# Performance work log

Hardware: AMD Instinct MI355X
Metric: run time of the kernel (lower is better)

## Reference

```python
import jax, jax.numpy as jnp
import numpy as np

DEGREE = 3        # self.degree = 3 in MGNN
K = 3             # Chebyshev/polynomial order of the GCN
BANDWIDTH = 512.0 # Gaussian kernel bandwidth (~2*d so adj spans (0,1])
B, N, D_IN = 2, 4096, 256
D_OUT = 64        # 2*D_OUT == 128 == linear output dim


def _bspline(t, degree):
    """Cox-de Boor recursive B-spline basis N_{0,degree}(t), elementwise,
    uniform knots on [0,1]. t: [B,N,N] adjacency values."""
    knots = np.linspace(0.0, 1.0, degree + 2)  # static python floats
    basis = [jnp.where((t >= knots[i]) & (t < knots[i + 1]), 1.0, 0.0).astype(t.dtype)
             for i in range(degree + 1)]
    for k in range(1, degree + 1):
        basis = [
            (t - knots[i]) / (knots[i + k] - knots[i]) * basis[i]
            + (knots[i + k + 1] - t) / (knots[i + k + 1] - knots[i + 1]) * basis[i + 1]
            for i in range(degree + 1 - k)
        ]
    return basis[0]


def _wavelet(t, degree):
    # spline wavelet: difference of dilated/shifted B-splines
    return _bspline(2.0 * t, degree) - _bspline(2.0 * t - 1.0, degree)


def _graph_construction(x, bandwidth):
    # Gaussian-kernel dense adjacency per batch element: [B,N,N], values in (0,1]
    sq = jnp.sum(x * x, axis=-1)                                   # [B,N]
    d2 = sq[:, :, None] + sq[:, None, :] - 2.0 * jnp.einsum('bnd,bmd->bnm', x, x)
    d2 = jnp.maximum(d2, 0.0)
    return jnp.exp(-d2 / bandwidth)


def _gcn(x, kernel, Wk):
    # out = sum_k (kernel^k x) W_k ; Wk: [K, D_IN, D_OUT]
    h = x
    out = jnp.einsum('bnd,do->bno', h, Wk[0])
    for k in range(1, Wk.shape[0]):
        h = jnp.einsum('bnm,bmd->bnd', kernel, h)
        out = out + jnp.einsum('bnd,do->bno', h, Wk[k])
    return out


def setup_inputs() -> dict:
    key = jax.random.key(0)
    k0, k1, k2, k3 = jax.random.split(key, 4)
    x = jax.random.normal(k0, (B, N, D_IN), dtype=jnp.float32)
    Wk = jax.random.normal(k1, (K, D_IN, D_OUT), dtype=jnp.float32) * 0.05
    W_lin = jax.random.normal(k2, (D_IN, 2 * D_OUT), dtype=jnp.float32) * 0.05
    b_lin = jnp.zeros((2 * D_OUT,), dtype=jnp.float32)
    return {"x": x, "Wk": Wk, "W_lin": W_lin, "b_lin": b_lin}


def reference(x, Wk, W_lin, b_lin):
    adj = _graph_construction(x, BANDWIDTH)       # [B,N,N]
    b_kernel = _bspline(adj, DEGREE)              # [B,N,N]
    w_kernel = _wavelet(adj, DEGREE)              # [B,N,N]
    gcn1 = _gcn(x, b_kernel, Wk)                  # [B,N,D_OUT]
    gcn2 = _gcn(x, w_kernel, Wk)                  # [B,N,D_OUT]
    akgcn = jnp.concatenate([gcn1, gcn2], axis=-1)        # [B,N,2*D_OUT]
    akgcn = jax.nn.relu(akgcn + x @ W_lin + b_lin)        # residual + relu
    return akgcn.reshape(akgcn.shape[0], -1)              # flatten last two dims
```

## Files before the change

kernel.cpp:

```cpp
#include <hip/hip_runtime.h>
#include <hip/hip_bf16.h>

typedef __hip_bfloat16 bf16;
typedef float v4f __attribute__((ext_vector_type(4)));
typedef short v8s __attribute__((ext_vector_type(8)));

typedef const __attribute__((address_space(1))) void gvoid;
typedef __attribute__((address_space(3))) void lvoid;

__device__ __forceinline__ void async16(const void* g, void* l) {
  __builtin_amdgcn_global_load_lds((gvoid*)g, (lvoid*)l, 16, 0, 0);
}

__device__ __forceinline__ unsigned short f2bf(float v) {
  __hip_bfloat16 h = __float2bfloat16(v);
  return *(unsigned short*)&h;
}
__device__ __forceinline__ float bflo(unsigned dw) {
  unsigned u = dw << 16;
  return *(float*)&u;
}
__device__ __forceinline__ float bfhi(unsigned dw) {
  unsigned u = dw & 0xffff0000u;
  return *(float*)&u;
}

__device__ __forceinline__ float b3(float u) {
  u = fminf(fmaxf(u, 0.f), 4.f);
  float t1 = fmaxf(u - 1.f, 0.f);
  float t2 = fmaxf(u - 2.f, 0.f);
  float t3 = fmaxf(u - 3.f, 0.f);
  float c0 = u * u * u;
  float c1 = t1 * t1 * t1;
  float c2 = t2 * t2 * t2;
  float c3 = t3 * t3 * t3;
  return (c0 - 4.f * c1 + 6.f * c2 - 4.f * c3) * (1.f / 6.f);
}

template <int NI, int BK>
__device__ __forceinline__ void mfma_loop(const bf16* __restrict__ A,
                                          const bf16* __restrict__ B, int lda,
                                          int ldb, int kLen, bf16* As, bf16* Bs,
                                          v4f acc[4][NI]) {
  const int tid = threadIdx.x;
  const int wave = tid >> 6;
  const int lane = tid & 63;
  const int quad = lane >> 4;
  const int r16 = lane & 15;
  const int wm = (wave >> 1) * 64;
  const int wn = (wave & 1) * (NI * 16);
  constexpr int CPR = BK / 8;
  constexpr int AQ = 128 * CPR / 256;
  constexpr int BQ = NI * 32 * CPR / 256;
  char* AsC = (char*)As;
  char* BsC = (char*)Bs;
  for (int kk = 0; kk < kLen; kk += BK) {
#pragma unroll
    for (int q = 0; q < AQ; ++q) {
      const int ch = tid + 256 * q;
      const int r = ch / CPR, c = (ch % CPR) * 8;
      async16(A + (size_t)r * lda + kk + c, AsC + q * 4096 + wave * 1024);
    }
#pragma unroll
    for (int q = 0; q < BQ; ++q) {
      const int ch = tid + 256 * q;
      const int r = ch / CPR, c = (ch % CPR) * 8;
      async16(B + (size_t)r * ldb + kk + c, BsC + q * 4096 + wave * 1024);
    }
    __syncthreads();
#pragma unroll
    for (int ks = 0; ks < BK / 32; ++ks) {
      v8s af[4], bfr[NI];
#pragma unroll
      for (int mi = 0; mi < 4; ++mi)
        af[mi] =
            *(const v8s*)(As + (wm + mi * 16 + r16) * BK + ks * 32 + quad * 8);
#pragma unroll
      for (int ni = 0; ni < NI; ++ni)
        bfr[ni] =
            *(const v8s*)(Bs + (wn + ni * 16 + r16) * BK + ks * 32 + quad * 8);
#pragma unroll
      for (int mi = 0; mi < 4; ++mi)
#pragma unroll
        for (int ni = 0; ni < NI; ++ni)
          acc[mi][ni] = __builtin_amdgcn_mfma_f32_16x16x32_bf16(
              af[mi], bfr[ni], acc[mi][ni], 0, 0, 0);
    }
    __syncthreads();
  }
}

__global__ void prep(const float* __restrict__ x, bf16* __restrict__ U,
                     float* __restrict__ sq) {
  const int n = blockIdx.x, b = blockIdx.y, t = threadIdx.x;
  const size_t row = (size_t)b * 4096 + n;
  float v = x[row * 256 + t];
  U[row * 1280 + t] = __float2bfloat16(v);
  float s = v * v;
#pragma unroll
  for (int o = 32; o > 0; o >>= 1) s += __shfl_down(s, o, 64);
  __shared__ float ls[4];
  if ((t & 63) == 0) ls[t >> 6] = s;
  __syncthreads();
  if (t == 0) sq[row] = ls[0] + ls[1] + ls[2] + ls[3];
}

__global__ void transk(const float* __restrict__ src, bf16* __restrict__ dst) {
  __shared__ float tile[64][65];
  const int z = blockIdx.z;
  const float* s = src + (size_t)z * 4096 * 256;
  bf16* d = dst + (size_t)z * 256 * 4096;
  const int n0 = blockIdx.x * 64, d0 = blockIdx.y * 64;
  const int tx = threadIdx.x & 31, ty = threadIdx.x >> 5;
#pragma unroll
  for (int i = 0; i < 8; ++i) {
    const int r = ty + i * 8;
    const float2 v = *(const float2*)(s + (size_t)(n0 + r) * 256 + d0 + tx * 2);
    tile[r][tx * 2] = v.x;
    tile[r][tx * 2 + 1] = v.y;
  }
  __syncthreads();
#pragma unroll
  for (int i = 0; i < 8; ++i) {
    const int c = ty + i * 8;
    __hip_bfloat162 p;
    p.x = __float2bfloat16(tile[tx * 2][c]);
    p.y = __float2bfloat16(tile[tx * 2 + 1][c]);
    *(__hip_bfloat162*)(d + (size_t)(d0 + c) * 4096 + n0 + tx * 2) = p;
  }
}

__global__ void wbig(const float* __restrict__ Wk, const float* __restrict__ Wl,
                     bf16* __restrict__ WbT) {
  int idx = blockIdx.x * 256 + threadIdx.x;
  if (idx >= 128 * 1280) return;
  int j = idx / 1280, k = idx % 1280;
  int o = j & 63;
  float v = 0.f;
  if (k < 256)
    v = Wk[k * 64 + o] + Wl[k * 128 + j];
  else if (k < 512)
    v = (j < 64) ? Wk[16384 + (k - 256) * 64 + o] : 0.f;
  else if (k < 768)
    v = (j < 64) ? Wk[32768 + (k - 512) * 64 + o] : 0.f;
  else if (k < 1024)
    v = (j >= 64) ? Wk[16384 + (k - 768) * 64 + o] : 0.f;
  else
    v = (j >= 64) ? Wk[32768 + (k - 1024) * 64 + o] : 0.f;
  WbT[idx] = __float2bfloat16(v);
}

__global__ __launch_bounds__(256, 2) void gemm_s(const bf16* __restrict__ U,
                                                 const float* __restrict__ sq,
                                                 bf16* __restrict__ kmat) {
  __shared__ __align__(16) bf16 As[128 * 64];
  __shared__ __align__(16) bf16 Bs[128 * 64];
  __shared__ unsigned lut[2048];
  const int tid = threadIdx.x;
  for (int i = tid; i < 2048; i += 256) {
    float t = (i + 0.5f) * (1.f / 2048.f);
    float bv = b3(4.f * t);
    float wv = b3(8.f * t) - b3(8.f * t - 4.f);
    lut[i] = (unsigned)f2bf(bv) | ((unsigned)f2bf(wv) << 16);
  }
  const int z = blockIdx.z;
  const bf16* A = U + (size_t)z * 4096 * 1280 + (size_t)blockIdx.x * 128 * 1280;
  const bf16* B = U + (size_t)z * 4096 * 1280 + (size_t)blockIdx.y * 128 * 1280;
  v4f acc[4][4];
#pragma unroll
  for (int a = 0; a < 4; ++a)
#pragma unroll
    for (int b2 = 0; b2 < 4; ++b2) acc[a][b2] = (v4f){0.f, 0.f, 0.f, 0.f};
  mfma_loop<4, 64>(A, B, 1280, 1280, 256, As, Bs, acc);
  const int wave = tid >> 6, lane = tid & 63;
  const int quad = lane >> 4, r16 = lane & 15;
  const int wm = (wave >> 1) * 64, wn = (wave & 1) * 64;
  const float* sqr = sq + (size_t)z * 4096;
  unsigned short* bk = (unsigned short*)(kmat + (size_t)(z * 2) * 4096 * 4096);
  unsigned short* wk = bk + (size_t)4096 * 4096;
  const int i0 = blockIdx.x * 128 + wm + quad * 4;
  const int j0 = blockIdx.y * 128 + wn + r16;
  const int par = lane & 1;
  const int jc = j0 - par;
  float sqj[4];
#pragma unroll
  for (int ni = 0; ni < 4; ++ni) sqj[ni] = sqr[j0 + ni * 16];
  const float c = -1.4426950408889634f / 512.f;
#pragma unroll
  for (int mi = 0; mi < 4; ++mi) {
#pragma unroll
    for (int ni = 0; ni < 4; ++ni) {
      unsigned pv[4];
#pragma unroll
      for (int r = 0; r < 4; ++r) {
        float s = acc[mi][ni][r];
        float d2 = fmaxf(sqr[i0 + mi * 16 + r] + sqj[ni] - 2.f * s, 0.f);
        float t = __builtin_amdgcn_exp2f(d2 * c);
        int idx = (int)fminf(t * 2048.f, 2047.f);
        pv[r] = lut[idx];
      }
      unsigned ov[4];
#pragma unroll
      for (int r = 0; r < 4; ++r) ov[r] = __shfl_xor((int)pv[r], 1, 64);
#pragma unroll
      for (int rr = 0; rr < 2; ++rr) {
        const int r = par * 2 + rr;
        const unsigned a = pv[r], b2 = ov[r];
        const unsigned lo = par ? b2 : a;
        const unsigned hi = par ? a : b2;
        const unsigned bkd = (lo & 0xffffu) | (hi << 16);
        const unsigned wkd = (lo >> 16) | (hi & 0xffff0000u);
        const int i = i0 + mi * 16 + r;
        const size_t off = (size_t)i * 4096 + jc + ni * 16;
        *(unsigned*)(bk + off) = bkd;
        *(unsigned*)(wk + off) = wkd;
      }
    }
  }
}

__global__ __launch_bounds__(256, 4) void gemm_h(const bf16* __restrict__ kmat,
                                                 const bf16* __restrict__ BtBase,
                                                 bf16* __restrict__ hpart,
                                                 int btShift) {
  __shared__ __align__(16) bf16 As[128 * 64];
  __shared__ __align__(16) bf16 Bs[128 * 64];
  const int bz = blockIdx.z;
  const int z = bz >> 2, split = bz & 3;
  const int kk0 = split * 1024;
  const bf16* A =
      kmat + (size_t)z * 4096 * 4096 + (size_t)blockIdx.x * 128 * 4096 + kk0;
  const bf16* B = BtBase + (size_t)(z >> btShift) * 256 * 4096 +
                  (size_t)blockIdx.y * 128 * 4096 + kk0;
  v4f acc[4][4];
#pragma unroll
  for (int a = 0; a < 4; ++a)
#pragma unroll
    for (int b2 = 0; b2 < 4; ++b2) acc[a][b2] = (v4f){0.f, 0.f, 0.f, 0.f};
  mfma_loop<4, 64>(A, B, 4096, 4096, 1024, As, Bs, acc);
  const int tid = threadIdx.x, wave = tid >> 6, lane = tid & 63;
  const int quad = lane >> 4, r16 = lane & 15;
  const int wm = (wave >> 1) * 64, wn = (wave & 1) * 64;
  bf16* H = hpart + ((size_t)split * 4 + z) * 4096 * 256;
  const int i0 = blockIdx.x * 128 + wm + quad * 4;
  const int j0 = blockIdx.y * 128 + wn + r16;
  const int par = lane & 1;
  const int jc = j0 - par;
#pragma unroll
  for (int mi = 0; mi < 4; ++mi) {
#pragma unroll
    for (int ni = 0; ni < 4; ++ni) {
      unsigned pv[4];
#pragma unroll
      for (int r = 0; r < 4; ++r) pv[r] = (unsigned)f2bf(acc[mi][ni][r]);
      unsigned ov[4];
#pragma unroll
      for (int r = 0; r < 4; ++r) ov[r] = __shfl_xor((int)pv[r], 1, 64);
#pragma unroll
      for (int rr = 0; rr < 2; ++rr) {
        const int r = par * 2 + rr;
        const unsigned a = pv[r], b2 = ov[r];
        const unsigned lo = par ? b2 : a;
        const unsigned hi = par ? a : b2;
        const int i = i0 + mi * 16 + r;
        *(unsigned*)(H + (size_t)i * 256 + jc + ni * 16) = lo | (hi << 16);
      }
    }
  }
}

__global__ void reduceT(const bf16* __restrict__ hpart, bf16* __restrict__ U,
                        bf16* __restrict__ hT, int uoffBase) {
  __shared__ float tile[64][65];
  const int z = blockIdx.z;
  const int b = z >> 1, kern = z & 1;
  const int uoff = uoffBase + kern * 512;
  const int n0 = blockIdx.x * 64, d0 = blockIdx.y * 64;
  const int tx = threadIdx.x & 31, ty = threadIdx.x >> 5;
  const size_t sstride = (size_t)4 * 4096 * 256;
  const bf16* s0 = hpart + (size_t)z * 4096 * 256;
#pragma unroll
  for (int i = 0; i < 8; ++i) {
    const int r = ty + i * 8;
    const size_t off = (size_t)(n0 + r) * 256 + d0 + tx * 2;
    float vx = 0.f, vy = 0.f;
#pragma unroll
    for (int k = 0; k < 4; ++k) {
      const unsigned dw = *(const unsigned*)(s0 + k * sstride + off);
      vx += bflo(dw);
      vy += bfhi(dw);
    }
    tile[r][tx * 2] = vx;
    tile[r][tx * 2 + 1] = vy;
    __hip_bfloat162 p;
    p.x = __float2bfloat16(vx);
    p.y = __float2bfloat16(vy);
    *(__hip_bfloat162*)(U + (size_t)(b * 4096 + n0 + r) * 1280 + uoff + d0 +
                        tx * 2) = p;
  }
  if (hT) {
    __syncthreads();
#pragma unroll
    for (int i = 0; i < 8; ++i) {
      const int c = ty + i * 8;
      __hip_bfloat162 p;
      p.x = __float2bfloat16(tile[tx * 2][c]);
      p.y = __float2bfloat16(tile[tx * 2 + 1][c]);
      *(__hip_bfloat162*)(hT + (size_t)z * 256 * 4096 + (size_t)(d0 + c) * 4096 +
                          n0 + tx * 2) = p;
    }
  }
}

__global__ __launch_bounds__(256, 4) void gemm_proj(
    const bf16* __restrict__ U, const bf16* __restrict__ WbT,
    const float* __restrict__ blin, float* __restrict__ out) {
  __shared__ __align__(16) bf16 As[128 * 64];
  __shared__ __align__(16) bf16 Bs[64 * 64];
  const bf16* A = U + (size_t)blockIdx.x * 128 * 1280;
  const bf16* B = WbT + (size_t)blockIdx.y * 64 * 1280;
  v4f acc[4][2];
#pragma unroll
  for (int a = 0; a < 4; ++a)
#pragma unroll
    for (int b2 = 0; b2 < 2; ++b2) acc[a][b2] = (v4f){0.f, 0.f, 0.f, 0.f};
  mfma_loop<2, 64>(A, B, 1280, 1280, 1280, As, Bs, acc);
  const int tid = threadIdx.x, wave = tid >> 6, lane = tid & 63;
  const int quad = lane >> 4, r16 = lane & 15;
  const int wm = (wave >> 1) * 64, wn = (wave & 1) * 32;
  const int i0 = blockIdx.x * 128 + wm + quad * 4;
  const int j0 = blockIdx.y * 64 + wn + r16;
#pragma unroll
  for (int mi = 0; mi < 4; ++mi)
#pragma unroll
    for (int r = 0; r < 4; ++r) {
      const int i = i0 + mi * 16 + r;
#pragma unroll
      for (int ni = 0; ni < 2; ++ni) {
        const int j = j0 + ni * 16;
        out[(size_t)i * 128 + j] = fmaxf(acc[mi][ni][r] + blin[j], 0.f);
      }
    }
}

extern "C" void kernel_launch(void* const* d_in, const int* in_sizes, int n_in,
                              void* d_out, int out_size, void* d_ws,
                              size_t ws_size, hipStream_t stream) {
  const float* x = (const float*)d_in[0];
  const float* Wk = (const float*)d_in[1];
  const float* Wlin = (const float*)d_in[2];
  const float* blin = (const float*)d_in[3];
  float* out = (float*)d_out;
  char* w = (char*)d_ws;
  bf16* kmat = (bf16*)(w);
  bf16* hpart = (bf16*)(w + 134217728);
  bf16* h1T = (bf16*)(w + 201326592);
  bf16* xhT = (bf16*)(w + 209715200);
  bf16* U = (bf16*)(w + 213909504);
  bf16* WbT = (bf16*)(w + 234881024);
  float* sqv = (float*)(w + 235208704);

  prep<<<dim3(4096, 2), 256, 0, stream>>>(x, U, sqv);
  transk<<<dim3(64, 4, 2), 256, 0, stream>>>(x, xhT);
  wbig<<<dim3(640), 256, 0, stream>>>(Wk, Wlin, WbT);
  gemm_s<<<dim3(32, 32, 2), 256, 0, stream>>>(U, sqv, kmat);
  gemm_h<<<dim3(32, 2, 16), 256, 0, stream>>>(kmat, xhT, hpart, 1);
  reduceT<<<dim3(64, 4, 4), 256, 0, stream>>>(hpart, U, h1T, 256);
  gemm_h<<<dim3(32, 2, 16), 256, 0, stream>>>(kmat, h1T, hpart, 0);
  reduceT<<<dim3(64, 4, 4), 256, 0, stream>>>(hpart, U, nullptr, 512);
  gemm_proj<<<dim3(64, 2), 256, 0, stream>>>(U, WbT, blin, out);
}
```

Before: 243.7 us.

## Store B-spline and wavelet kernels as packed 8-bit codes and dequantize in GEMM

The adjacency-derived B-spline and wavelet kernel matrices were stored as two bf16 planes. They are now quantized to 8-bit codes, packed into one 16-bit word per element, and written as a single plane. The propagation GEMM loads these words through registers, unpacks and dequantizes them to bf16, and writes them to LDS. This halves kernel-matrix traffic in both the writing kernel and the two reading GEMMs. The costs are coarser precision in the kernel values, extra ALU work per loaded element, and losing the asynchronous LDS load for the A operand.

```diff
diff --git a/kernel.cpp b/kernel.cpp
--- a/kernel.cpp
+++ b/kernel.cpp
@@ -4,6 +4,7 @@
 typedef __hip_bfloat16 bf16;
 typedef float v4f __attribute__((ext_vector_type(4)));
 typedef short v8s __attribute__((ext_vector_type(8)));
+typedef unsigned u32;
 
 typedef const __attribute__((address_space(1))) void gvoid;
 typedef __attribute__((address_space(3))) void lvoid;
@@ -16,12 +17,12 @@
   __hip_bfloat16 h = __float2bfloat16(v);
   return *(unsigned short*)&h;
 }
-__device__ __forceinline__ float bflo(unsigned dw) {
-  unsigned u = dw << 16;
+__device__ __forceinline__ float bflo(u32 dw) {
+  u32 u = dw << 16;
   return *(float*)&u;
 }
-__device__ __forceinline__ float bfhi(unsigned dw) {
-  unsigned u = dw & 0xffff0000u;
+__device__ __forceinline__ float bfhi(u32 dw) {
+  u32 u = dw & 0xffff0000u;
   return *(float*)&u;
 }
 
@@ -152,16 +153,18 @@
 
 __global__ __launch_bounds__(256, 2) void gemm_s(const bf16* __restrict__ U,
                                                  const float* __restrict__ sq,
-                                                 bf16* __restrict__ kmat) {
+                                                 unsigned short* __restrict__ kbw) {
   __shared__ __align__(16) bf16 As[128 * 64];
   __shared__ __align__(16) bf16 Bs[128 * 64];
-  __shared__ unsigned lut[2048];
+  __shared__ u32 lut[2048];
   const int tid = threadIdx.x;
   for (int i = tid; i < 2048; i += 256) {
     float t = (i + 0.5f) * (1.f / 2048.f);
     float bv = b3(4.f * t);
     float wv = b3(8.f * t) - b3(8.f * t - 4.f);
-    lut[i] = (unsigned)f2bf(bv) | ((unsigned)f2bf(wv) << 16);
+    u32 bq = (u32)fminf(bv * 382.5f + 0.5f, 255.f);
+    u32 wq = (u32)fminf((wv + 2.f / 3.f) * 191.25f + 0.5f, 255.f);
+    lut[i] = bq | (wq << 8);
   }
   const int z = blockIdx.z;
   const bf16* A = U + (size_t)z * 4096 * 1280 + (size_t)blockIdx.x * 128 * 1280;
@@ -176,8 +179,7 @@
   const int quad = lane >> 4, r16 = lane & 15;
   const int wm = (wave >> 1) * 64, wn = (wave & 1) * 64;
   const float* sqr = sq + (size_t)z * 4096;
-  unsigned short* bk = (unsigned short*)(kmat + (size_t)(z * 2) * 4096 * 4096);
-  unsigned short* wk = bk + (size_t)4096 * 4096;
+  unsigned short* ks = kbw + (size_t)z * 4096 * 4096;
   const int i0 = blockIdx.x * 128 + wm + quad * 4;
   const int j0 = blockIdx.y * 128 + wn + r16;
   const int par = lane & 1;
@@ -190,7 +192,7 @@
   for (int mi = 0; mi < 4; ++mi) {
 #pragma unroll
     for (int ni = 0; ni < 4; ++ni) {
-      unsigned pv[4];
+      u32 pv[4];
 #pragma unroll
       for (int r = 0; r < 4; ++r) {
         float s = acc[mi][ni][r];
@@ -199,48 +201,103 @@
         int idx = (int)fminf(t * 2048.f, 2047.f);
         pv[r] = lut[idx];
       }
-      unsigned ov[4];
+      u32 ov[4];
 #pragma unroll
       for (int r = 0; r < 4; ++r) ov[r] = __shfl_xor((int)pv[r], 1, 64);
 #pragma unroll
       for (int rr = 0; rr < 2; ++rr) {
         const int r = par * 2 + rr;
-        const unsigned a = pv[r], b2 = ov[r];
-        const unsigned lo = par ? b2 : a;
-        const unsigned hi = par ? a : b2;
-        const unsigned bkd = (lo & 0xffffu) | (hi << 16);
-        const unsigned wkd = (lo >> 16) | (hi & 0xffff0000u);
+        const u32 a = pv[r], b2 = ov[r];
+        const u32 lo = par ? b2 : a;
+        const u32 hi = par ? a : b2;
         const int i = i0 + mi * 16 + r;
         const size_t off = (size_t)i * 4096 + jc + ni * 16;
-        *(unsigned*)(bk + off) = bkd;
-        *(unsigned*)(wk + off) = wkd;
+        *(u32*)(ks + off) = (lo & 0xffffu) | (hi << 16);
       }
     }
   }
 }
 
-__global__ __launch_bounds__(256, 4) void gemm_h(const bf16* __restrict__ kmat,
-                                                 const bf16* __restrict__ BtBase,
-                                                 bf16* __restrict__ hpart,
-                                                 int btShift) {
+__global__ __launch_bounds__(256, 4) void gemm_h(
+    const unsigned short* __restrict__ kbw, const bf16* __restrict__ BtBase,
+    bf16* __restrict__ hpart, int btShift) {
   __shared__ __align__(16) bf16 As[128 * 64];
   __shared__ __align__(16) bf16 Bs[128 * 64];
   const int bz = blockIdx.z;
   const int z = bz >> 2, split = bz & 3;
+  const int batch = z >> 1, kern = z & 1;
   const int kk0 = split * 1024;
-  const bf16* A =
-      kmat + (size_t)z * 4096 * 4096 + (size_t)blockIdx.x * 128 * 4096 + kk0;
+  const unsigned short* A = kbw + (size_t)batch * 4096 * 4096 +
+                            (size_t)blockIdx.x * 128 * 4096 + kk0;
   const bf16* B = BtBase + (size_t)(z >> btShift) * 256 * 4096 +
                   (size_t)blockIdx.y * 128 * 4096 + kk0;
-  v4f acc[4][4];
-#pragma unroll
-  for (int a = 0; a < 4; ++a)
-#pragma unroll
-    for (int b2 = 0; b2 < 4; ++b2) acc[a][b2] = (v4f){0.f, 0.f, 0.f, 0.f};
-  mfma_loop<4, 64>(A, B, 4096, 4096, 1024, As, Bs, acc);
-  const int tid = threadIdx.x, wave = tid >> 6, lane = tid & 63;
+  const float ksc = kern ? (4.f / 3.f / 255.f) : (2.f / 3.f / 255.f);
+  const float kof = kern ? (-2.f / 3.f) : 0.f;
+  const int sh0 = kern * 8, sh1 = 16 + kern * 8;
+  const int tid = threadIdx.x;
+  const int wave = tid >> 6, lane = tid & 63;
   const int quad = lane >> 4, r16 = lane & 15;
   const int wm = (wave >> 1) * 64, wn = (wave & 1) * 64;
+  char* BsC = (char*)Bs;
+  char* AsC = (char*)As;
+  v4f acc[4][4];
+#pragma unroll
+  for (int a = 0; a < 4; ++a)
+#pragma unroll
+    for (int b2 = 0; b2 < 4; ++b2) acc[a][b2] = (v4f){0.f, 0.f, 0.f, 0.f};
+  for (int kk = 0; kk < 1024; kk += 64) {
+    uint4 ad[4];
+#pragma unroll
+    for (int q = 0; q < 4; ++q) {
+      const int ch = q * 256 + tid;
+      const int r = ch >> 3, c8 = (ch & 7) * 8;
+      ad[q] = *(const uint4*)(A + (size_t)r * 4096 + kk + c8);
+    }
+#pragma unroll
+    for (int q = 0; q < 4; ++q) {
+      const int ch = tid + 256 * q;
+      const int r = ch / 8, cB = (ch % 8) * 8;
+      async16(B + (size_t)r * 4096 + kk + cB, BsC + q * 4096 + wave * 1024);
+    }
+#pragma unroll
+    for (int q = 0; q < 4; ++q) {
+      u32 o[4];
+      const u32 d0 = ad[q].x, d1 = ad[q].y, d2 = ad[q].z, d3 = ad[q].w;
+      const u32 din[4] = {d0, d1, d2, d3};
+#pragma unroll
+      for (int d = 0; d < 4; ++d) {
+        const u32 dw = din[d];
+        float f0 = (float)((dw >> sh0) & 0xffu) * ksc + kof;
+        float f1 = (float)((dw >> sh1) & 0xffu) * ksc + kof;
+        o[d] = __builtin_amdgcn_perm(__float_as_uint(f1), __float_as_uint(f0),
+                                     0x07060302u);
+      }
+      const int ch = q * 256 + tid;
+      uint4 ov4;
+      ov4.x = o[0]; ov4.y = o[1]; ov4.z = o[2]; ov4.w = o[3];
+      *(uint4*)(AsC + ch * 16) = ov4;
+    }
+    __syncthreads();
+#pragma unroll
+    for (int ks = 0; ks < 2; ++ks) {
+      v8s af[4], bfr[4];
+#pragma unroll
+      for (int mi = 0; mi < 4; ++mi)
+        af[mi] =
+            *(const v8s*)(As + (wm + mi * 16 + r16) * 64 + ks * 32 + quad * 8);
+#pragma unroll
+      for (int ni = 0; ni < 4; ++ni)
+        bfr[ni] =
+            *(const v8s*)(Bs + (wn + ni * 16 + r16) * 64 + ks * 32 + quad * 8);
+#pragma unroll
+      for (int mi = 0; mi < 4; ++mi)
+#pragma unroll
+        for (int ni = 0; ni < 4; ++ni)
+          acc[mi][ni] = __builtin_amdgcn_mfma_f32_16x16x32_bf16(
+              af[mi], bfr[ni], acc[mi][ni], 0, 0, 0);
+    }
+    __syncthreads();
+  }
   bf16* H = hpart + ((size_t)split * 4 + z) * 4096 * 256;
   const int i0 = blockIdx.x * 128 + wm + quad * 4;
   const int j0 = blockIdx.y * 128 + wn + r16;
@@ -250,20 +307,20 @@
   for (int mi = 0; mi < 4; ++mi) {
 #pragma unroll
     for (int ni = 0; ni < 4; ++ni) {
-      unsigned pv[4];
-#pragma unroll
-      for (int r = 0; r < 4; ++r) pv[r] = (unsigned)f2bf(acc[mi][ni][r]);
-      unsigned ov[4];
+      u32 pv[4];
+#pragma unroll
+      for (int r = 0; r < 4; ++r) pv[r] = (u32)f2bf(acc[mi][ni][r]);
+      u32 ov[4];
 #pragma unroll
       for (int r = 0; r < 4; ++r) ov[r] = __shfl_xor((int)pv[r], 1, 64);
 #pragma unroll
       for (int rr = 0; rr < 2; ++rr) {
         const int r = par * 2 + rr;
-        const unsigned a = pv[r], b2 = ov[r];
-        const unsigned lo = par ? b2 : a;
-        const unsigned hi = par ? a : b2;
+        const u32 a = pv[r], b2 = ov[r];
+        const u32 lo = par ? b2 : a;
+        const u32 hi = par ? a : b2;
         const int i = i0 + mi * 16 + r;
-        *(unsigned*)(H + (size_t)i * 256 + jc + ni * 16) = lo | (hi << 16);
+        *(u32*)(H + (size_t)i * 256 + jc + ni * 16) = lo | (hi << 16);
       }
     }
   }
@@ -286,7 +343,7 @@
     float vx = 0.f, vy = 0.f;
 #pragma unroll
     for (int k = 0; k < 4; ++k) {
-      const unsigned dw = *(const unsigned*)(s0 + k * sstride + off);
+      const u32 dw = *(const u32*)(s0 + k * sstride + off);
       vx += bflo(dw);
       vy += bfhi(dw);
     }
@@ -352,21 +409,21 @@
   const float* blin = (const float*)d_in[3];
   float* out = (float*)d_out;
   char* w = (char*)d_ws;
-  bf16* kmat = (bf16*)(w);
-  bf16* hpart = (bf16*)(w + 134217728);
-  bf16* h1T = (bf16*)(w + 201326592);
-  bf16* xhT = (bf16*)(w + 209715200);
-  bf16* U = (bf16*)(w + 213909504);
-  bf16* WbT = (bf16*)(w + 234881024);
-  float* sqv = (float*)(w + 235208704);
+  unsigned short* kbw = (unsigned short*)(w);
+  bf16* hpart = (bf16*)(w + 67108864);
+  bf16* h1T = (bf16*)(w + 100663296);
+  bf16* xhT = (bf16*)(w + 109051904);
+  bf16* U = (bf16*)(w + 113246208);
+  bf16* WbT = (bf16*)(w + 134217728);
+  float* sqv = (float*)(w + 134545408);
 
   prep<<<dim3(4096, 2), 256, 0, stream>>>(x, U, sqv);
   transk<<<dim3(64, 4, 2), 256, 0, stream>>>(x, xhT);
   wbig<<<dim3(640), 256, 0, stream>>>(Wk, Wlin, WbT);
-  gemm_s<<<dim3(32, 32, 2), 256, 0, stream>>>(U, sqv, kmat);
-  gemm_h<<<dim3(32, 2, 16), 256, 0, stream>>>(kmat, xhT, hpart, 1);
+  gemm_s<<<dim3(32, 32, 2), 256, 0, stream>>>(U, sqv, kbw);
+  gemm_h<<<dim3(32, 2, 16), 256, 0, stream>>>(kbw, xhT, hpart, 1);
   reduceT<<<dim3(64, 4, 4), 256, 0, stream>>>(hpart, U, h1T, 256);
-  gemm_h<<<dim3(32, 2, 16), 256, 0, stream>>>(kmat, h1T, hpart, 0);
+  gemm_h<<<dim3(32, 2, 16), 256, 0, stream>>>(kbw, h1T, hpart, 0);
   reduceT<<<dim3(64, 4, 4), 256, 0, stream>>>(hpart, U, nullptr, 512);
   gemm_proj<<<dim3(64, 2), 256, 0, stream>>>(U, WbT, blin, out);
 }
```

Result: slower. 256.3 us (+5.2%).
